# Kernel optimization log

Hardware: AMD Instinct MI355X
Metric: run time of the kernel (lower is better)

The kernel has to match this reference:

```python
import jax, jax.numpy as jnp
import numpy as np

D_MODEL = 1024
N_HEADS = 16
D_K = D_MODEL // N_HEADS  # 64, also d_v
B, S = 8, 1024


def setup_inputs() -> dict:
    key = jax.random.key(0)
    ks = jax.random.split(key, 12)
    sc = 1.0 / np.sqrt(D_MODEL)
    inp = {
        "q": jax.random.normal(ks[0], (B, S, D_MODEL), jnp.float32),
        "k": jax.random.normal(ks[1], (B, S, D_MODEL), jnp.float32),
        "v": jax.random.normal(ks[2], (B, S, D_MODEL), jnp.float32),
        # per-head projection weights stacked over heads; torch Linear stores [out,in]
        "Wq": jax.random.normal(ks[3], (N_HEADS, D_K, D_MODEL), jnp.float32) * sc,
        "bq": jax.random.normal(ks[4], (N_HEADS, D_K), jnp.float32) * sc,
        "Wk": jax.random.normal(ks[5], (N_HEADS, D_K, D_MODEL), jnp.float32) * sc,
        "bk": jax.random.normal(ks[6], (N_HEADS, D_K), jnp.float32) * sc,
        "Wv": jax.random.normal(ks[7], (N_HEADS, D_K, D_MODEL), jnp.float32) * sc,
        "bv": jax.random.normal(ks[8], (N_HEADS, D_K), jnp.float32) * sc,
        "Wf": jax.random.normal(ks[9], (D_MODEL, D_MODEL), jnp.float32) * sc,
        "bf": jax.random.normal(ks[10], (D_MODEL,), jnp.float32) * sc,
    }
    return inp


def reference(q, k, v, Wq, bq, Wk, bk, Wv, bv, Wf, bf):
    temper = jnp.asarray(D_K ** 0.5, q.dtype)
    # per-head linear projections, all heads at once: [b,s,h,dk]
    qh = jnp.einsum('bsd,hkd->bhsk', q, Wq) + bq[None, :, None, :]
    kh = jnp.einsum('bsd,hkd->bhsk', k, Wk) + bk[None, :, None, :]
    vh = jnp.einsum('bsd,hkd->bhsk', v, Wv) + bv[None, :, None, :]
    # scaled dot-product scores [b,h,s,s]
    scores = jnp.einsum('bhik,bhjk->bhij', qh, kh) / temper
    # faithful scalar-equality mask: positions exactly equal to mask (=0) -> -inf
    scores = jnp.where(scores == 0.0, -jnp.inf, scores)
    attn = jax.nn.softmax(scores, axis=-1)
    out = jnp.einsum('bhij,bhjv->bhiv', attn, vh)  # [b,h,s,dv]
    # concat heads (head order matches torch.cat over ModuleList)
    out = out.transpose(0, 2, 1, 3).reshape(out.shape[0], out.shape[2], -1)  # [b,s,d_model]
    return out @ Wf.T + bf
```

## Files before the change

kernel.cpp:

```cpp
#include <hip/hip_runtime.h>
#include <hip/hip_bf16.h>


#define D_MODEL_ 1024
#define NH_ 16
#define DK_ 64
#define B_ 8
#define S_ 1024
#define M_ (B_ * S_)

typedef __hip_bfloat16 bf16;
typedef __attribute__((ext_vector_type(8))) short short8;
typedef __attribute__((ext_vector_type(4))) short short4_t;
typedef __attribute__((ext_vector_type(4))) float f32x4;

typedef const __attribute__((address_space(1))) unsigned int* gas_u32p;
typedef __attribute__((address_space(3))) unsigned int* las_u32p;

__device__ __forceinline__ short f2bs(float x) {
  bf16 h = __float2bfloat16(x);
  return *reinterpret_cast<short*>(&h);
}

__global__ __launch_bounds__(256)
void conv_w4(const float* __restrict__ w0, const float* __restrict__ w1,
             const float* __restrict__ w2, const float* __restrict__ w3,
             bf16* __restrict__ out) {
  const float* src = (blockIdx.z == 0) ? w0 : (blockIdx.z == 1) ? w1
                   : (blockIdx.z == 2) ? w2 : w3;
  size_t i = ((size_t)blockIdx.x * 256 + threadIdx.x) * 8;
  f32x4 a = *(const f32x4*)(src + i);
  f32x4 b = *(const f32x4*)(src + i + 4);
  short8 s;
  s[0] = f2bs(a[0]); s[1] = f2bs(a[1]); s[2] = f2bs(a[2]); s[3] = f2bs(a[3]);
  s[4] = f2bs(b[0]); s[5] = f2bs(b[1]); s[6] = f2bs(b[2]); s[7] = f2bs(b[3]);
  *(short8*)((short*)out + (size_t)blockIdx.z * 1024 * 1024 + i) = s;
}

template<int BN, int AF32>
__device__ __forceinline__ void gemm_body(const void* __restrict__ A,
                                          const bf16* __restrict__ Wb,
                                          const float* __restrict__ bias,
                                          void* __restrict__ C,
                                          int cMode, float cscale, int m0, int n0)
{
  __shared__ short As[2][128 * 32];
  __shared__ short Bs[2][BN * 32];
  const int tid = threadIdx.x;
  const int lane = tid & 63;
  const int w = tid >> 6;
  const int l15 = lane & 15, quad = lane >> 4;
  const int wm = (w >> 1) * 64, wn = (w & 1) * (BN / 2);
  const int rsl = (quad ^ ((l15 >> 1) & 3)) * 8;

  constexpr int NPB = BN / 32;

  f32x4 au[4], av[4];
  short8 ab[4];
  short8 bb[NPB];

  auto loadA = [&](int k0) {
    if (AF32) {
      const float* Af = (const float*)A;
#pragma unroll
      for (int p = 0; p < 4; ++p) {
        int c = p * 256 + tid;
        int r = c >> 3, kc = (c & 7) * 8;
        const float* g = Af + (size_t)(m0 + r) * 1024 + k0 + kc;
        au[p] = *(const f32x4*)g;
        av[p] = *(const f32x4*)(g + 4);
      }
    } else {
      const bf16* Ab = (const bf16*)A;
#pragma unroll
      for (int p = 0; p < 4; ++p) {
        int c = p * 256 + tid;
        int r = c >> 3, kc = (c & 7) * 8;
        ab[p] = *(const short8*)((const short*)Ab + (size_t)(m0 + r) * 1024 + k0 + kc);
      }
    }
  };
  auto writeA = [&]() {
#pragma unroll
    for (int p = 0; p < 4; ++p) {
      int c = p * 256 + tid;
      int r = c >> 3, kc = (c & 7) * 8;
      int s = (c & 3) ^ ((r >> 1) & 3);
      if (AF32) {
        short8 sv;
        sv[0] = f2bs(au[p][0]); sv[1] = f2bs(au[p][1]); sv[2] = f2bs(au[p][2]); sv[3] = f2bs(au[p][3]);
        sv[4] = f2bs(av[p][0]); sv[5] = f2bs(av[p][1]); sv[6] = f2bs(av[p][2]); sv[7] = f2bs(av[p][3]);
        *(short8*)&As[kc >> 5][r * 32 + s * 8] = sv;
      } else {
        *(short8*)&As[kc >> 5][r * 32 + s * 8] = ab[p];
      }
    }
  };
  auto loadB = [&](int k0) {
#pragma unroll
    for (int p = 0; p < NPB; ++p) {
      int c = p * 256 + tid;
      int r = c >> 3, kc = (c & 7) * 8;
      bb[p] = *(const short8*)((const short*)Wb + (size_t)(n0 + r) * 1024 + k0 + kc);
    }
  };
  auto writeB = [&]() {
#pragma unroll
    for (int p = 0; p < NPB; ++p) {
      int c = p * 256 + tid;
      int r = c >> 3, kc = (c & 7) * 8;
      int s = (c & 3) ^ ((r >> 1) & 3);
      *(short8*)&Bs[kc >> 5][r * 32 + s * 8] = bb[p];
    }
  };

  f32x4 acc[4][NPB];
#pragma unroll
  for (int i = 0; i < 4; ++i)
#pragma unroll
    for (int j = 0; j < NPB; ++j)
      acc[i][j] = (f32x4){0.f, 0.f, 0.f, 0.f};

  loadA(0);
  loadB(0);

  for (int k0 = 0; k0 < 1024; k0 += 64) {
    __builtin_amdgcn_s_barrier();
    writeA();
    writeB();
    asm volatile("s_waitcnt lgkmcnt(0)" ::: "memory");
    __builtin_amdgcn_s_barrier();
    __builtin_amdgcn_sched_barrier(0);

    if (k0 + 64 < 1024) {
      loadA(k0 + 64);
      loadB(k0 + 64);
    }

#pragma unroll
    for (int kk = 0; kk < 2; ++kk) {
      short8 af[4], bfv[NPB];
#pragma unroll
      for (int t = 0; t < 4; ++t)
        af[t]  = *(short8*)&As[kk][(wm + t * 16 + l15) * 32 + rsl];
#pragma unroll
      for (int t = 0; t < NPB; ++t)
        bfv[t] = *(short8*)&Bs[kk][(wn + t * 16 + l15) * 32 + rsl];
#pragma unroll
      for (int mt = 0; mt < 4; ++mt)
#pragma unroll
        for (int nt = 0; nt < NPB; ++nt)
          acc[mt][nt] = __builtin_amdgcn_mfma_f32_16x16x32_bf16(af[mt], bfv[nt], acc[mt][nt], 0, 0, 0);
    }
  }

  if (cMode == 2) {
    bf16* vt = (bf16*)C;
    const int bidx = m0 >> 10;
    const int sbase = (m0 & 1023) + wm;
#pragma unroll
    for (int nt = 0; nt < NPB; ++nt) {
      int n = n0 + wn + nt * 16 + l15;
      float bv = bias[n];
#pragma unroll
      for (int mt = 0; mt < 4; ++mt) {
        int s = sbase + mt * 16 + quad * 4;
        short4_t pk;
#pragma unroll
        for (int r = 0; r < 4; ++r) pk[r] = f2bs((acc[mt][nt][r] + bv) * cscale);
        *(short4_t*)((short*)vt + ((size_t)bidx * 1024 + n) * 1024 + s) = pk;
      }
    }
  } else {
#pragma unroll
    for (int nt = 0; nt < NPB; ++nt) {
      int col = n0 + wn + nt * 16 + l15;
      float bv = bias[col];
#pragma unroll
      for (int mt = 0; mt < 4; ++mt)
#pragma unroll
        for (int r = 0; r < 4; ++r) {
          int row = m0 + wm + mt * 16 + quad * 4 + r;
          float val = (acc[mt][nt][r] + bv) * cscale;
          if (cMode == 1) ((float*)C)[(size_t)row * 1024 + col] = val;
          else ((bf16*)C)[(size_t)row * 1024 + col] = __float2bfloat16(val);
        }
    }
  }
}

__global__ __launch_bounds__(256)
void gemm_proj(const float* __restrict__ q, const float* __restrict__ k,
               const float* __restrict__ v, const bf16* __restrict__ wq,
               const bf16* __restrict__ wk, const bf16* __restrict__ wv,
               const float* __restrict__ bq, const float* __restrict__ bk,
               const float* __restrict__ bv, void* __restrict__ cq,
               void* __restrict__ ck, void* __restrict__ cv)
{
  const int z = blockIdx.z;
  const float* A = (z == 0) ? q : (z == 1) ? k : v;
  const bf16* W  = (z == 0) ? wq : (z == 1) ? wk : wv;
  const float* bb = (z == 0) ? bq : (z == 1) ? bk : bv;
  void* C = (z == 0) ? cq : (z == 1) ? ck : cv;
  int cMode = (z == 2) ? 2 : 0;
  float cscale = (z == 0) ? 0.18033688011112042f : 1.0f;
  gemm_body<128, 1>(A, W, bb, C, cMode, cscale, blockIdx.x * 128, blockIdx.y * 128);
}

__global__ __launch_bounds__(256)
void gemm_final(const bf16* __restrict__ A, const bf16* __restrict__ W,
                const float* __restrict__ bias, void* __restrict__ C)
{
  gemm_body<64, 0>(A, W, bias, C, 1, 1.0f, blockIdx.x * 128, blockIdx.y * 64);
}

__global__ __launch_bounds__(256)
void attn_mfma(const bf16* __restrict__ QH, const bf16* __restrict__ KH,
               const bf16* __restrict__ VT, bf16* __restrict__ AO)
{
  __shared__ short Ks[2][64 * 32];
  __shared__ short Vs[2][64 * 32];
  __shared__ short Ps[4][16 * 72];
  const int tid = threadIdx.x;
  const int lane = tid & 63;
  const int w = tid >> 6;
  const int l15 = lane & 15, quad = lane >> 4;
  const int q0 = blockIdx.x * 64;
  const int h = blockIdx.y, b = blockIdx.z;
  const size_t base = ((size_t)b * S_) * D_MODEL_ + (size_t)h * DK_;
  const size_t vtb  = (((size_t)b * NH_ + h) * DK_) * (size_t)S_;
  short* myPs = Ps[w];

  const int srow = 16 * w + (lane >> 2);
  const int lchunk = (lane & 3) * 8;
  const int wslot = ((lane & 3) ^ ((lane >> 3) & 3)) * 8;
  const int rsl = (quad ^ ((l15 >> 1) & 3)) * 8;

  short8 kreg[2], vreg[2];
  auto loadKV = [&](int j0) {
#pragma unroll
    for (int sub = 0; sub < 2; ++sub) {
      kreg[sub] = *(const short8*)((const short*)KH + base + (size_t)(j0 + srow) * D_MODEL_ + sub * 32 + lchunk);
      vreg[sub] = *(const short8*)((const short*)VT + vtb + (size_t)srow * S_ + j0 + sub * 32 + lchunk);
    }
  };
  auto writeKV = [&]() {
#pragma unroll
    for (int sub = 0; sub < 2; ++sub) {
      *(short8*)&Ks[sub][(srow & 63) * 32 + wslot] = kreg[sub];
      *(short8*)&Vs[sub][(srow & 63) * 32 + wslot] = vreg[sub];
    }
  };

  short8 qa[2];
#pragma unroll
  for (int ks = 0; ks < 2; ++ks)
    qa[ks] = *(const short8*)((const short*)QH + base + (size_t)(q0 + w * 16 + l15) * D_MODEL_ + ks * 32 + quad * 8);

  float li = 0.f;
  f32x4 oacc[4];
#pragma unroll
  for (int nt = 0; nt < 4; ++nt) oacc[nt] = (f32x4){0.f, 0.f, 0.f, 0.f};

  loadKV(0);

  for (int j0 = 0; j0 < S_; j0 += 64) {
    __builtin_amdgcn_s_barrier();
    writeKV();
    asm volatile("s_waitcnt lgkmcnt(0)" ::: "memory");
    __builtin_amdgcn_s_barrier();
    __builtin_amdgcn_sched_barrier(0);

    if (j0 + 64 < S_) loadKV(j0 + 64);

    short8 kb[4][2], vb[4][2];
#pragma unroll
    for (int nt = 0; nt < 4; ++nt)
#pragma unroll
      for (int ks = 0; ks < 2; ++ks) {
        kb[nt][ks] = *(short8*)&Ks[ks][(nt * 16 + l15) * 32 + rsl];
        vb[nt][ks] = *(short8*)&Vs[ks][(nt * 16 + l15) * 32 + rsl];
      }

    f32x4 sacc[4];
#pragma unroll
    for (int nt = 0; nt < 4; ++nt) sacc[nt] = (f32x4){0.f, 0.f, 0.f, 0.f};
    __builtin_amdgcn_s_setprio(1);
#pragma unroll
    for (int nt = 0; nt < 4; ++nt)
#pragma unroll
      for (int ks = 0; ks < 2; ++ks)
        sacc[nt] = __builtin_amdgcn_mfma_f32_16x16x32_bf16(kb[nt][ks], qa[ks], sacc[nt], 0, 0, 0);
    __builtin_amdgcn_s_setprio(0);

    float p[4][4];
#pragma unroll
    for (int nt = 0; nt < 4; ++nt) {
#pragma unroll
      for (int r = 0; r < 4; ++r) {
        float x = sacc[nt][r];
        float e = exp2f(x);
        p[nt][r] = (x == 0.0f) ? 0.0f : e;
      }
      li += (p[nt][0] + p[nt][1]) + (p[nt][2] + p[nt][3]);
    }

#pragma unroll
    for (int nt = 0; nt < 4; ++nt) {
      short4_t pk;
#pragma unroll
      for (int r = 0; r < 4; ++r) pk[r] = f2bs(p[nt][r]);
      *(short4_t*)&myPs[l15 * 72 + nt * 16 + quad * 4] = pk;
    }

    __threadfence_block();

    short8 pa[2];
#pragma unroll
    for (int ks = 0; ks < 2; ++ks)
      pa[ks] = *(short8*)&myPs[l15 * 72 + ks * 32 + quad * 8];
    __builtin_amdgcn_s_setprio(1);
#pragma unroll
    for (int nt = 0; nt < 4; ++nt)
#pragma unroll
      for (int ks = 0; ks < 2; ++ks)
        oacc[nt] = __builtin_amdgcn_mfma_f32_16x16x32_bf16(pa[ks], vb[nt][ks], oacc[nt], 0, 0, 0);
    __builtin_amdgcn_s_setprio(0);
  }

  li += __shfl_xor(li, 16, 64);
  li += __shfl_xor(li, 32, 64);
  float lr[4];
#pragma unroll
  for (int r = 0; r < 4; ++r) lr[r] = __shfl(li, quad * 4 + r, 64);
#pragma unroll
  for (int r = 0; r < 4; ++r) {
    float inv = (lr[r] > 0.f) ? 1.0f / lr[r] : 0.f;
    int q = q0 + w * 16 + quad * 4 + r;
#pragma unroll
    for (int nt = 0; nt < 4; ++nt)
      AO[base + (size_t)q * D_MODEL_ + nt * 16 + l15] = __float2bfloat16(oacc[nt][r] * inv);
  }
}

extern "C" void kernel_launch(void* const* d_in, const int* in_sizes, int n_in,
                              void* d_out, int out_size, void* d_ws, size_t ws_size,
                              hipStream_t stream) {
  (void)in_sizes; (void)n_in; (void)out_size;
  const float* q  = (const float*)d_in[0];
  const float* k  = (const float*)d_in[1];
  const float* v  = (const float*)d_in[2];
  const float* Wq = (const float*)d_in[3];
  const float* bq = (const float*)d_in[4];
  const float* Wk = (const float*)d_in[5];
  const float* bk = (const float*)d_in[6];
  const float* Wv = (const float*)d_in[7];
  const float* bv = (const float*)d_in[8];
  const float* Wf = (const float*)d_in[9];
  const float* bF = (const float*)d_in[10];

  const size_t MB = (size_t)1024 * 1024;
  char* ws = (char*)d_ws;
  bf16* wqb = (bf16*)(ws);
  bf16* wkb = (bf16*)(ws + 2 * MB);
  bf16* wvb = (bf16*)(ws + 4 * MB);
  bf16* wfb = (bf16*)(ws + 6 * MB);
  bf16* vt  = (bf16*)(ws + 8 * MB);
  bf16* qh  = (bf16*)d_out;
  bf16* kh  = (bf16*)((char*)d_out + 16 * MB);

  const bool bigws = ws_size >= (size_t)40 * MB;
  bf16* aob = bigws ? (bf16*)(ws + 24 * MB) : qh;
  bf16* fin = bigws ? aob : (bf16*)(ws + 8 * MB);

  dim3 blk(256);

  conv_w4<<<dim3(512, 1, 4), blk, 0, stream>>>(Wq, Wk, Wv, Wf, wqb);

  gemm_proj<<<dim3(M_ / 128, D_MODEL_ / 128, 3), blk, 0, stream>>>(
      q, k, v, wqb, wkb, wvb, bq, bk, bv, qh, kh, vt);

  attn_mfma<<<dim3(S_ / 64, NH_, B_), blk, 0, stream>>>(qh, kh, vt, aob);

  if (!bigws)
    hipMemcpyAsync(ws + 8 * MB, d_out, 16 * MB, hipMemcpyDeviceToDevice, stream);

  gemm_final<<<dim3(M_ / 128, D_MODEL_ / 64), blk, 0, stream>>>(fin, wfb, bF, d_out);
}
```

Before: 318.5 us.

## Double query rows per attention block and enlarge final GEMM tile

The attention kernel now handles 128 query rows per block, with each wave processing two 16-row groups. Each K/V tile staged in shared memory is therefore reused across twice as many queries, which halves global K/V traffic and the number of barriers per query. The final projection GEMM moves from 128x64 to 128x128 tiles. In exchange both kernels use more registers and launch fewer blocks (1024 attention blocks, 512 GEMM blocks), which may lower occupancy and latency hiding.

```diff
diff --git a/kernel.cpp b/kernel.cpp
--- a/kernel.cpp
+++ b/kernel.cpp
@@ -211,7 +211,7 @@
 void gemm_final(const bf16* __restrict__ A, const bf16* __restrict__ W,
                 const float* __restrict__ bias, void* __restrict__ C)
 {
-  gemm_body<64, 0>(A, W, bias, C, 1, 1.0f, blockIdx.x * 128, blockIdx.y * 64);
+  gemm_body<128, 0>(A, W, bias, C, 1, 1.0f, blockIdx.x * 128, blockIdx.y * 128);
 }
 
 __global__ __launch_bounds__(256)
@@ -220,16 +220,15 @@
 {
   __shared__ short Ks[2][64 * 32];
   __shared__ short Vs[2][64 * 32];
-  __shared__ short Ps[4][16 * 72];
+  __shared__ short Ps[4][2][16 * 72];
   const int tid = threadIdx.x;
   const int lane = tid & 63;
   const int w = tid >> 6;
   const int l15 = lane & 15, quad = lane >> 4;
-  const int q0 = blockIdx.x * 64;
+  const int q0 = blockIdx.x * 128;
   const int h = blockIdx.y, b = blockIdx.z;
   const size_t base = ((size_t)b * S_) * D_MODEL_ + (size_t)h * DK_;
   const size_t vtb  = (((size_t)b * NH_ + h) * DK_) * (size_t)S_;
-  short* myPs = Ps[w];
 
   const int srow = 16 * w + (lane >> 2);
   const int lchunk = (lane & 3) * 8;
@@ -252,15 +251,20 @@
     }
   };
 
-  short8 qa[2];
-#pragma unroll
-  for (int ks = 0; ks < 2; ++ks)
-    qa[ks] = *(const short8*)((const short*)QH + base + (size_t)(q0 + w * 16 + l15) * D_MODEL_ + ks * 32 + quad * 8);
-
-  float li = 0.f;
-  f32x4 oacc[4];
-#pragma unroll
-  for (int nt = 0; nt < 4; ++nt) oacc[nt] = (f32x4){0.f, 0.f, 0.f, 0.f};
+  short8 qa[2][2];
+#pragma unroll
+  for (int g = 0; g < 2; ++g)
+#pragma unroll
+    for (int ks = 0; ks < 2; ++ks)
+      qa[g][ks] = *(const short8*)((const short*)QH + base
+                   + (size_t)(q0 + w * 32 + g * 16 + l15) * D_MODEL_ + ks * 32 + quad * 8);
+
+  float li[2] = {0.f, 0.f};
+  f32x4 oacc[2][4];
+#pragma unroll
+  for (int g = 0; g < 2; ++g)
+#pragma unroll
+    for (int nt = 0; nt < 4; ++nt) oacc[g][nt] = (f32x4){0.f, 0.f, 0.f, 0.f};
 
   loadKV(0);
 
@@ -282,64 +286,72 @@
         vb[nt][ks] = *(short8*)&Vs[ks][(nt * 16 + l15) * 32 + rsl];
       }
 
-    f32x4 sacc[4];
-#pragma unroll
-    for (int nt = 0; nt < 4; ++nt) sacc[nt] = (f32x4){0.f, 0.f, 0.f, 0.f};
-    __builtin_amdgcn_s_setprio(1);
-#pragma unroll
-    for (int nt = 0; nt < 4; ++nt)
+#pragma unroll
+    for (int g = 0; g < 2; ++g) {
+      f32x4 sacc[4];
+#pragma unroll
+      for (int nt = 0; nt < 4; ++nt) sacc[nt] = (f32x4){0.f, 0.f, 0.f, 0.f};
+      __builtin_amdgcn_s_setprio(1);
+#pragma unroll
+      for (int nt = 0; nt < 4; ++nt)
+#pragma unroll
+        for (int ks = 0; ks < 2; ++ks)
+          sacc[nt] = __builtin_amdgcn_mfma_f32_16x16x32_bf16(kb[nt][ks], qa[g][ks], sacc[nt], 0, 0, 0);
+      __builtin_amdgcn_s_setprio(0);
+
+      float p[4][4];
+#pragma unroll
+      for (int nt = 0; nt < 4; ++nt) {
+#pragma unroll
+        for (int r = 0; r < 4; ++r) {
+          float x = sacc[nt][r];
+          float e = exp2f(x);
+          p[nt][r] = (x == 0.0f) ? 0.0f : e;
+        }
+        li[g] += (p[nt][0] + p[nt][1]) + (p[nt][2] + p[nt][3]);
+      }
+
+      short* myPs = Ps[w][g];
+#pragma unroll
+      for (int nt = 0; nt < 4; ++nt) {
+        short4_t pk;
+#pragma unroll
+        for (int r = 0; r < 4; ++r) pk[r] = f2bs(p[nt][r]);
+        *(short4_t*)&myPs[l15 * 72 + nt * 16 + quad * 4] = pk;
+      }
+
+      __threadfence_block();
+
+      short8 pa[2];
 #pragma unroll
       for (int ks = 0; ks < 2; ++ks)
-        sacc[nt] = __builtin_amdgcn_mfma_f32_16x16x32_bf16(kb[nt][ks], qa[ks], sacc[nt], 0, 0, 0);
-    __builtin_amdgcn_s_setprio(0);
-
-    float p[4][4];
-#pragma unroll
-    for (int nt = 0; nt < 4; ++nt) {
-#pragma unroll
-      for (int r = 0; r < 4; ++r) {
-        float x = sacc[nt][r];
-        float e = exp2f(x);
-        p[nt][r] = (x == 0.0f) ? 0.0f : e;
-      }
-      li += (p[nt][0] + p[nt][1]) + (p[nt][2] + p[nt][3]);
-    }
-
-#pragma unroll
-    for (int nt = 0; nt < 4; ++nt) {
-      short4_t pk;
-#pragma unroll
-      for (int r = 0; r < 4; ++r) pk[r] = f2bs(p[nt][r]);
-      *(short4_t*)&myPs[l15 * 72 + nt * 16 + quad * 4] = pk;
-    }
-
-    __threadfence_block();
-
-    short8 pa[2];
-#pragma unroll
-    for (int ks = 0; ks < 2; ++ks)
-      pa[ks] = *(short8*)&myPs[l15 * 72 + ks * 32 + quad * 8];
-    __builtin_amdgcn_s_setprio(1);
-#pragma unroll
-    for (int nt = 0; nt < 4; ++nt)
-#pragma unroll
-      for (int ks = 0; ks < 2; ++ks)
-        oacc[nt] = __builtin_amdgcn_mfma_f32_16x16x32_bf16(pa[ks], vb[nt][ks], oacc[nt], 0, 0, 0);
-    __builtin_amdgcn_s_setprio(0);
+        pa[ks] = *(short8*)&myPs[l15 * 72 + ks * 32 + quad * 8];
+      __builtin_amdgcn_s_setprio(1);
+#pragma unroll
+      for (int nt = 0; nt < 4; ++nt)
+#pragma unroll
+        for (int ks = 0; ks < 2; ++ks)
+          oacc[g][nt] = __builtin_amdgcn_mfma_f32_16x16x32_bf16(pa[ks], vb[nt][ks], oacc[g][nt], 0, 0, 0);
+      __builtin_amdgcn_s_setprio(0);
+    }
   }
 
-  li += __shfl_xor(li, 16, 64);
-  li += __shfl_xor(li, 32, 64);
-  float lr[4];
-#pragma unroll
-  for (int r = 0; r < 4; ++r) lr[r] = __shfl(li, quad * 4 + r, 64);
-#pragma unroll
-  for (int r = 0; r < 4; ++r) {
-    float inv = (lr[r] > 0.f) ? 1.0f / lr[r] : 0.f;
-    int q = q0 + w * 16 + quad * 4 + r;
-#pragma unroll
-    for (int nt = 0; nt < 4; ++nt)
-      AO[base + (size_t)q * D_MODEL_ + nt * 16 + l15] = __float2bfloat16(oacc[nt][r] * inv);
+#pragma unroll
+  for (int g = 0; g < 2; ++g) {
+    float lg = li[g];
+    lg += __shfl_xor(lg, 16, 64);
+    lg += __shfl_xor(lg, 32, 64);
+    float lr[4];
+#pragma unroll
+    for (int r = 0; r < 4; ++r) lr[r] = __shfl(lg, quad * 4 + r, 64);
+#pragma unroll
+    for (int r = 0; r < 4; ++r) {
+      float inv = (lr[r] > 0.f) ? 1.0f / lr[r] : 0.f;
+      int qq = q0 + w * 32 + g * 16 + quad * 4 + r;
+#pragma unroll
+      for (int nt = 0; nt < 4; ++nt)
+        AO[base + (size_t)qq * D_MODEL_ + nt * 16 + l15] = __float2bfloat16(oacc[g][nt][r] * inv);
+    }
   }
 }
 
@@ -380,10 +392,10 @@
   gemm_proj<<<dim3(M_ / 128, D_MODEL_ / 128, 3), blk, 0, stream>>>(
       q, k, v, wqb, wkb, wvb, bq, bk, bv, qh, kh, vt);
 
-  attn_mfma<<<dim3(S_ / 64, NH_, B_), blk, 0, stream>>>(qh, kh, vt, aob);
+  attn_mfma<<<dim3(S_ / 128, NH_, B_), blk, 0, stream>>>(qh, kh, vt, aob);
 
   if (!bigws)
     hipMemcpyAsync(ws + 8 * MB, d_out, 16 * MB, hipMemcpyDeviceToDevice, stream);
 
-  gemm_final<<<dim3(M_ / 128, D_MODEL_ / 64), blk, 0, stream>>>(fin, wfb, bF, d_out);
-}
+  gemm_final<<<dim3(M_ / 128, D_MODEL_ / 128), blk, 0, stream>>>(fin, wfb, bF, d_out);
+}
```

Result: faster. 307.9 us (-3.3%).
